# Optimization experiments

Measured on AMD Instinct MI355X. Metric: run time of the kernel, lower is better.

The kernel has to match this reference:

```python
import jax, jax.numpy as jnp
import numpy as np

B, L, C = 2048, 2048, 16
F = L // 2                 # num_freqs = 1024
H = 4 * F                  # multi_factor * num_freqs = 4096
P = int(len(np.unique(L // np.arange(1, F + 1))))  # n patch sizes = 88
SCALE = 0.02
NOISE_EPS = 0.01


def setup_inputs() -> dict:
    key = jax.random.key(0)
    ks = jax.random.split(key, 10)
    return {
        "x": jax.random.normal(ks[0], (B, L, C), jnp.float32),
        "w_start": SCALE * jax.random.normal(ks[1], (C, 1), jnp.float32),
        "b_start": SCALE * jax.random.normal(ks[2], (1,), jnp.float32),
        "w1": SCALE * jax.random.normal(ks[3], (2, F, H), jnp.float32),
        "b1": SCALE * jax.random.normal(ks[4], (2, H), jnp.float32),
        "w2": SCALE * jax.random.normal(ks[5], (2, H, F), jnp.float32),
        "b2": SCALE * jax.random.normal(ks[6], (2, F), jnp.float32),
        "w_gate": SCALE * jax.random.normal(ks[7], (F, P), jnp.float32),
        "w_noise": SCALE * jax.random.normal(ks[8], (F, P), jnp.float32),
        "noise_z": jax.random.normal(ks[9], (B, P), jnp.float32),
        "top_k": 3,
    }


def reference(x, w_start, b_start, w1, b1, w2, b2, w_gate, w_noise, noise_z, top_k):
    # start_fc: [B, L, C] -> [B, L, 1] -> [B, 1, L]
    v = (jnp.einsum("blc,co->blo", x, w_start) + b_start).transpose(0, 2, 1)
    # rfft (ortho), drop DC bin -> [B, 1, F] complex
    xf = jnp.fft.rfft(v, axis=-1, norm="ortho")[:, :, 1:]
    xr, xi = jnp.real(xf), jnp.imag(xf)
    # complex 2-layer MLP in frequency domain
    o1r = jax.nn.relu(jnp.einsum("bdi,io->bdo", xr, w1[0]) - jnp.einsum("bdi,io->bdo", xi, w1[1]) + b1[0])
    o1i = jax.nn.relu(jnp.einsum("bdi,io->bdo", xi, w1[0]) + jnp.einsum("bdi,io->bdo", xr, w1[1]) + b1[1])
    o2r = jnp.einsum("bdo,of->bdf", o1r, w2[0]) - jnp.einsum("bdo,of->bdf", o1i, w2[1]) + b2[0]
    o2i = jnp.einsum("bdo,of->bdf", o1i, w2[0]) + jnp.einsum("bdo,of->bdf", o1r, w2[1]) + b2[1]
    amp = jnp.sqrt(o2r * o2r + o2i * o2i)[:, 0, :]  # [B, F]
    # router logits with (training) noise injection
    clean_logits = amp @ w_gate                      # [B, P]
    noise_std = jax.nn.softplus(amp @ w_noise) + NOISE_EPS
    logits = clean_logits + noise_z * noise_std
    # top-k -> softmax over top-k -> scatter into sparse gates
    top_w, top_i = jax.lax.top_k(logits, top_k)
    top_w = jax.nn.softmax(top_w, axis=-1)
    rows = jnp.arange(logits.shape[0])[:, None]
    gates = jnp.zeros_like(logits).at[rows, top_i].set(top_w)
    return gates
```

## Files before the change

kernel.cpp:

```cpp
#include <hip/hip_runtime.h>
#include <hip/hip_bf16.h>
#include <math.h>

#define B_DIM 2048
#define L_DIM 2048
#define F_DIM 1024
#define H_DIM 4096
#define P_DIM 88

typedef unsigned short u16;
typedef short bf16x8 __attribute__((ext_vector_type(8)));
typedef float f32x4 __attribute__((ext_vector_type(4)));

__device__ __forceinline__ u16 f2bf(float x) {
    unsigned u = __float_as_uint(x);
    return (u16)((u + 0x7fffu + ((u >> 16) & 1u)) >> 16);
}
__device__ __forceinline__ float bf2f(u16 h) {
    return __uint_as_float(((unsigned)h) << 16);
}

__device__ __forceinline__ void gload_lds16(const void* g, void* l) {
    unsigned loff = (unsigned)(uintptr_t)l;
    __builtin_amdgcn_global_load_lds(
        reinterpret_cast<const __attribute__((address_space(1))) void*>(
            reinterpret_cast<uintptr_t>(g)),
        reinterpret_cast<__attribute__((address_space(3))) void*>(loff),
        16, 0, 0);
}

__global__ __launch_bounds__(256) void fft_kernel(
    const float* __restrict__ x, const float* __restrict__ w_start,
    const float* __restrict__ b_start, u16* __restrict__ A1)
{
    __shared__ float re[2048];
    __shared__ float im[2048];
    int b = blockIdx.x;

    const float4* wp = (const float4*)w_start;
    float4 w0 = wp[0], w1 = wp[1], w2 = wp[2], w3 = wp[3];
    float bs = b_start[0];

    for (int l = threadIdx.x; l < 2048; l += 256) {
        const float4* xp = (const float4*)(x + ((size_t)b * 2048 + l) * 16);
        float4 x0 = xp[0], x1 = xp[1], x2 = xp[2], x3 = xp[3];
        float acc = bs;
        acc += x0.x * w0.x + x0.y * w0.y + x0.z * w0.z + x0.w * w0.w;
        acc += x1.x * w1.x + x1.y * w1.y + x1.z * w1.z + x1.w * w1.w;
        acc += x2.x * w2.x + x2.y * w2.y + x2.z * w2.z + x2.w * w2.w;
        acc += x3.x * w3.x + x3.y * w3.y + x3.z * w3.z + x3.w * w3.w;
        unsigned j = __brev((unsigned)l) >> 21;
        re[j] = acc;
        im[j] = 0.f;
    }
    __syncthreads();

    for (int s = 1; s <= 11; s++) {
        int half = 1 << (s - 1);
        for (int t = threadIdx.x; t < 1024; t += 256) {
            int j = t & (half - 1);
            int base = (t >> (s - 1)) << s;
            float ang = -6.283185307179586f * (float)j / (float)(1 << s);
            float wr, wi;
            sincosf(ang, &wi, &wr);
            int i0 = base + j, i1 = i0 + half;
            float br = re[i1], bi = im[i1];
            float tr = br * wr - bi * wi;
            float ti = br * wi + bi * wr;
            float ar = re[i0], ai = im[i0];
            re[i0] = ar + tr; im[i0] = ai + ti;
            re[i1] = ar - tr; im[i1] = ai - ti;
        }
        __syncthreads();
    }

    const float sc = 0.022097086912079612f;
    u16* arow = A1 + (size_t)b * 4096;
    for (int t = threadIdx.x; t < 1024; t += 256) {
        float r = re[t + 1] * sc;
        float q = im[t + 1] * sc;
        u16 rh = f2bf(r); u16 rl = f2bf(r - bf2f(rh));
        u16 ih = f2bf(q); u16 il = f2bf(q - bf2f(ih));
        arow[t] = rh; arow[1024 + t] = rl;
        arow[2048 + t] = ih; arow[3072 + t] = il;
    }
}

__global__ __launch_bounds__(256) void conv_bt_kernel(
    const float* __restrict__ w, u16* __restrict__ BT, int Kc, int Nh)
{
    __shared__ float t0[32][33];
    __shared__ float t1[32][33];
    int k0 = blockIdx.x * 32, n0 = blockIdx.y * 32;
    int tx = threadIdx.x, ty = threadIdx.y;
    const float* w0 = w;
    const float* w1 = w + (size_t)Kc * Nh;

#pragma unroll
    for (int i = 0; i < 4; i++) {
        int k = k0 + ty + 8 * i;
        t0[ty + 8 * i][tx] = w0[(size_t)k * Nh + n0 + tx];
        t1[ty + 8 * i][tx] = w1[(size_t)k * Nh + n0 + tx];
    }
    __syncthreads();

    size_t K4 = 4 * (size_t)Kc;
    int k = k0 + tx;
#pragma unroll
    for (int i = 0; i < 4; i++) {
        int nl = ty + 8 * i;
        int n = n0 + nl;
        float br = t0[tx][nl];
        float bi = t1[tx][nl];
        u16 brh = f2bf(br); u16 brl = f2bf(br - bf2f(brh));
        float nbi = -bi;
        u16 nih = f2bf(nbi); u16 nil = f2bf(nbi - bf2f(nih));
        u16 pih = f2bf(bi);  u16 pil = f2bf(bi - bf2f(pih));
        u16* rowr = BT + (size_t)n * K4;
        rowr[0 * Kc + k] = brh; rowr[1 * Kc + k] = brl;
        rowr[2 * Kc + k] = nih; rowr[3 * Kc + k] = nil;
        u16* rowi = BT + (size_t)(Nh + n) * K4;
        rowi[0 * Kc + k] = pih; rowi[1 * Kc + k] = pil;
        rowi[2 * Kc + k] = brh; rowi[3 * Kc + k] = brl;
    }
}

extern __shared__ char smem8p[];

#define MFMA16(ACC0, ACC1, ACC2, ACC3, A0, A1, A2, A3)                          \
    ACC0[0] = __builtin_amdgcn_mfma_f32_16x16x32_bf16(A0, b0, ACC0[0], 0, 0, 0); \
    ACC0[1] = __builtin_amdgcn_mfma_f32_16x16x32_bf16(A0, b1, ACC0[1], 0, 0, 0); \
    ACC0[2] = __builtin_amdgcn_mfma_f32_16x16x32_bf16(A0, b2, ACC0[2], 0, 0, 0); \
    ACC0[3] = __builtin_amdgcn_mfma_f32_16x16x32_bf16(A0, b3, ACC0[3], 0, 0, 0); \
    ACC1[0] = __builtin_amdgcn_mfma_f32_16x16x32_bf16(A1, b0, ACC1[0], 0, 0, 0); \
    ACC1[1] = __builtin_amdgcn_mfma_f32_16x16x32_bf16(A1, b1, ACC1[1], 0, 0, 0); \
    ACC1[2] = __builtin_amdgcn_mfma_f32_16x16x32_bf16(A1, b2, ACC1[2], 0, 0, 0); \
    ACC1[3] = __builtin_amdgcn_mfma_f32_16x16x32_bf16(A1, b3, ACC1[3], 0, 0, 0); \
    ACC2[0] = __builtin_amdgcn_mfma_f32_16x16x32_bf16(A2, b0, ACC2[0], 0, 0, 0); \
    ACC2[1] = __builtin_amdgcn_mfma_f32_16x16x32_bf16(A2, b1, ACC2[1], 0, 0, 0); \
    ACC2[2] = __builtin_amdgcn_mfma_f32_16x16x32_bf16(A2, b2, ACC2[2], 0, 0, 0); \
    ACC2[3] = __builtin_amdgcn_mfma_f32_16x16x32_bf16(A2, b3, ACC2[3], 0, 0, 0); \
    ACC3[0] = __builtin_amdgcn_mfma_f32_16x16x32_bf16(A3, b0, ACC3[0], 0, 0, 0); \
    ACC3[1] = __builtin_amdgcn_mfma_f32_16x16x32_bf16(A3, b1, ACC3[1], 0, 0, 0); \
    ACC3[2] = __builtin_amdgcn_mfma_f32_16x16x32_bf16(A3, b2, ACC3[2], 0, 0, 0); \
    ACC3[3] = __builtin_amdgcn_mfma_f32_16x16x32_bf16(A3, b3, ACC3[3], 0, 0, 0);

template <int EPI, int SWZ>
__global__ __launch_bounds__(512, 2) void gemm8p(
    const u16* __restrict__ A, const u16* __restrict__ B,
    const float* __restrict__ biasL, const float* __restrict__ biasR,
    u16* __restrict__ OutU, float* __restrict__ P01, float* __restrict__ P23,
    int Kc, int KcLog, int NH, int nt)
{
    char* ldsA = smem8p;
    char* ldsB = smem8p + 65536;

    const int tid = threadIdx.x;
    const int w = tid >> 6, lane = tid & 63;
    const int wr = w >> 2, wc = w & 3;
    const int fr = lane & 15, kb = lane >> 4;

    int bx, by, z;
    if (SWZ) {
        int b = blockIdx.x;
        int xcd = b & 7, idx = b >> 3;
        bx = 4 * xcd + (idx & 3);
        by = idx >> 2;
        z = 0;
    } else {
        bx = blockIdx.x; by = blockIdx.y; z = blockIdx.z;
    }
    const int n0 = bx * 256, m0 = by * 256;
    const size_t K4 = 4 * (size_t)Kc;

    const int srow = tid >> 2;
    const int lk8 = (((tid & 3) ^ ((tid >> 3) & 3))) * 8;
    const int wb = (tid >> 6) * 1024;

    const int laneOff = fr * 64 + ((kb ^ ((fr >> 1) & 3)) << 4);

    f32x4 acc[8][4];
#pragma unroll
    for (int i = 0; i < 8; i++)
#pragma unroll
        for (int j = 0; j < 4; j++)
            acc[i][j] = (f32x4){0.f, 0.f, 0.f, 0.f};

    const int t0 = z * nt, te = t0 + nt;

    auto colA = [&](int t) {
        int k0 = t << 5;
        int seg = k0 >> KcLog, kk = k0 & (Kc - 1);
        int r3 = seg >= 3 ? seg - 3 : seg;
        int bs = seg >= 3 ? 2 : 0;
        return (bs + (r3 == 1 ? 1 : 0)) * Kc + kk;
    };
    auto colB = [&](int t) {
        int k0 = t << 5;
        int seg = k0 >> KcLog, kk = k0 & (Kc - 1);
        int r3 = seg >= 3 ? seg - 3 : seg;
        int bs = seg >= 3 ? 2 : 0;
        return (bs + (r3 == 2 ? 1 : 0)) * Kc + kk;
    };
    auto stageA = [&](int t) {
        const u16* src = A + (size_t)(m0 + srow) * K4 + colA(t) + lk8;
        char* dst = ldsA + (t & 3) * 16384 + wb;
        gload_lds16(src, dst);
        gload_lds16(src + (size_t)128 * K4, dst + 8192);
    };
    auto stageB = [&](int t) {
        const u16* src = B + (size_t)(n0 + srow) * K4 + colB(t) + lk8;
        char* dst = ldsB + (t & 3) * 16384 + wb;
        gload_lds16(src, dst);
        gload_lds16(src + (size_t)128 * K4, dst + 8192);
    };
    auto aBase = [&](int t) -> const char* {
        return ldsA + (t & 3) * 16384 + wr * 8192 + laneOff;
    };
    auto bBase = [&](int t) -> const char* {
        return ldsB + (t & 3) * 16384 + wc * 4096 + laneOff;
    };

    stageA(t0); stageB(t0);
    if (t0 + 1 < te) { stageA(t0 + 1); stageB(t0 + 1); }
    if (t0 + 1 < te) asm volatile("s_waitcnt vmcnt(4)" ::: "memory");
    else             asm volatile("s_waitcnt vmcnt(0)" ::: "memory");
    asm volatile("s_barrier" ::: "memory");

    bf16x8 b0, b1, b2, b3, a0, a1, a2, a3;
    {
        const char* aS = aBase(t0);
        const char* bS = bBase(t0);
        b0 = *(const bf16x8*)(bS + 0 * 1024);
        b1 = *(const bf16x8*)(bS + 1 * 1024);
        b2 = *(const bf16x8*)(bS + 2 * 1024);
        b3 = *(const bf16x8*)(bS + 3 * 1024);
        a0 = *(const bf16x8*)(aS + 0 * 1024);
        a1 = *(const bf16x8*)(aS + 1 * 1024);
        a2 = *(const bf16x8*)(aS + 2 * 1024);
        a3 = *(const bf16x8*)(aS + 3 * 1024);
    }

    for (int t = t0; t < te; ++t) {
        if (t + 2 < te) { stageA(t + 2); stageB(t + 2); }

        __builtin_amdgcn_s_setprio(1);
        MFMA16(acc[0], acc[1], acc[2], acc[3], a0, a1, a2, a3)
        __builtin_amdgcn_s_setprio(0);

        const char* aS = aBase(t);
        bf16x8 c0 = *(const bf16x8*)(aS + 4096 + 0 * 1024);
        bf16x8 c1 = *(const bf16x8*)(aS + 4096 + 1 * 1024);
        bf16x8 c2 = *(const bf16x8*)(aS + 4096 + 2 * 1024);
        bf16x8 c3 = *(const bf16x8*)(aS + 4096 + 3 * 1024);

        if (t + 2 < te) asm volatile("s_waitcnt vmcnt(4)" ::: "memory");
        else            asm volatile("s_waitcnt vmcnt(0)" ::: "memory");
        asm volatile("s_barrier" ::: "memory");

        __builtin_amdgcn_s_setprio(1);
        MFMA16(acc[4], acc[5], acc[6], acc[7], c0, c1, c2, c3)
        __builtin_amdgcn_s_setprio(0);

        if (t + 1 < te) {
            const char* aN = aBase(t + 1);
            const char* bN = bBase(t + 1);
            b0 = *(const bf16x8*)(bN + 0 * 1024);
            b1 = *(const bf16x8*)(bN + 1 * 1024);
            b2 = *(const bf16x8*)(bN + 2 * 1024);
            b3 = *(const bf16x8*)(bN + 3 * 1024);
            a0 = *(const bf16x8*)(aN + 0 * 1024);
            a1 = *(const bf16x8*)(aN + 1 * 1024);
            a2 = *(const bf16x8*)(aN + 2 * 1024);
            a3 = *(const bf16x8*)(aN + 3 * 1024);
        }
    }

    const int fq = kb;
#pragma unroll
    for (int nj = 0; nj < 4; nj++) {
        int n = n0 + wc * 64 + nj * 16 + fr;
        if (EPI == 0) {
            bool left = (n < NH);
            int nn = left ? n : (n - NH);
            float bias = left ? biasL[n] : biasR[nn];
#pragma unroll
            for (int mi = 0; mi < 8; mi++) {
                int mb = m0 + wr * 128 + mi * 16 + fq * 4;
#pragma unroll
                for (int r = 0; r < 4; r++) {
                    float val = fmaxf(acc[mi][nj][r] + bias, 0.f);
                    u16 h = f2bf(val);
                    u16 lo = f2bf(val - bf2f(h));
                    size_t rb = (size_t)(mb + r) * (4 * (size_t)NH);
                    if (left) { OutU[rb + nn] = h; OutU[rb + NH + nn] = lo; }
                    else { OutU[rb + 2 * (size_t)NH + nn] = h; OutU[rb + 3 * (size_t)NH + nn] = lo; }
                }
            }
        } else {
            const size_t PSZ = (size_t)2048 * 2048;
            float* Out = (z < 2) ? (P01 + (size_t)z * PSZ) : (P23 + (size_t)(z - 2) * PSZ);
#pragma unroll
            for (int mi = 0; mi < 8; mi++) {
                int mb = m0 + wr * 128 + mi * 16 + fq * 4;
#pragma unroll
                for (int r = 0; r < 4; r++)
                    Out[(size_t)(mb + r) * 2048 + n] = acc[mi][nj][r];
            }
        }
    }
}

__global__ __launch_bounds__(128) void router_kernel(
    const float* __restrict__ P01, const float* __restrict__ P23, int ZK,
    const float* __restrict__ b2,
    const float* __restrict__ w_gate, const float* __restrict__ w_noise,
    const float* __restrict__ noise_z, float* __restrict__ gates)
{
    __shared__ float s_amp[1024];
    __shared__ float s_logit[P_DIM];
    __shared__ int   s_idx[3];
    __shared__ float s_val[3];

    int b = blockIdx.x;
    const size_t PSZ = (size_t)2048 * 2048;
    const size_t roff = (size_t)b * 2048;

    for (int i = threadIdx.x; i < 1024; i += 128) {
        float orr = b2[i];
        float oii = b2[1024 + i];
        for (int zz = 0; zz < ZK; zz++) {
            const float* Pz = ((zz < 2) ? (P01 + (size_t)zz * PSZ)
                                        : (P23 + (size_t)(zz - 2) * PSZ)) + roff;
            orr += Pz[i];
            oii += Pz[1024 + i];
        }
        s_amp[i] = sqrtf(orr * orr + oii * oii);
    }
    __syncthreads();

    int p = threadIdx.x;
    if (p < P_DIM) {
        float cg = 0.f, cn = 0.f;
        for (int k = 0; k < 1024; k++) {
            float a = s_amp[k];
            cg = fmaf(a, w_gate[k * P_DIM + p], cg);
            cn = fmaf(a, w_noise[k * P_DIM + p], cn);
        }
        float ns = (cn > 20.f) ? cn : log1pf(expf(cn));
        ns += 0.01f;
        s_logit[p] = cg + noise_z[(size_t)b * P_DIM + p] * ns;
    }
    __syncthreads();

    if (threadIdx.x == 0) {
        int i0 = -1, i1 = -1, i2 = -1;
        float v0 = -1e30f, v1 = -1e30f, v2 = -1e30f;
        for (int i = 0; i < P_DIM; i++) {
            float t = s_logit[i];
            if (t > v0) { v0 = t; i0 = i; }
        }
        for (int i = 0; i < P_DIM; i++) {
            if (i == i0) continue;
            float t = s_logit[i];
            if (t > v1) { v1 = t; i1 = i; }
        }
        for (int i = 0; i < P_DIM; i++) {
            if (i == i0 || i == i1) continue;
            float t = s_logit[i];
            if (t > v2) { v2 = t; i2 = i; }
        }
        s_idx[0] = i0; s_idx[1] = i1; s_idx[2] = i2;
        s_val[0] = v0; s_val[1] = v1; s_val[2] = v2;
    }
    __syncthreads();

    if (p < P_DIM) {
        float m = s_val[0];
        float e0 = expf(s_val[0] - m);
        float e1 = expf(s_val[1] - m);
        float e2 = expf(s_val[2] - m);
        float inv = 1.f / (e0 + e1 + e2);
        float g = 0.f;
        if (p == s_idx[0]) g = e0 * inv;
        else if (p == s_idx[1]) g = e1 * inv;
        else if (p == s_idx[2]) g = e2 * inv;
        gates[(size_t)b * P_DIM + p] = g;
    }
}

extern "C" void kernel_launch(void* const* d_in, const int* in_sizes, int n_in,
                              void* d_out, int out_size, void* d_ws, size_t ws_size,
                              hipStream_t stream)
{
    const float* x       = (const float*)d_in[0];
    const float* w_start = (const float*)d_in[1];
    const float* b_start = (const float*)d_in[2];
    const float* w1      = (const float*)d_in[3];
    const float* b1      = (const float*)d_in[4];
    const float* w2      = (const float*)d_in[5];
    const float* b2      = (const float*)d_in[6];
    const float* w_gate  = (const float*)d_in[7];
    const float* w_noise = (const float*)d_in[8];
    const float* noise_z = (const float*)d_in[9];
    float* gates = (float*)d_out;

    const size_t MB = 1024 * 1024;
    char* base = (char*)d_ws;
    u16*  A1   = (u16*)(base + 16 * MB);
    u16*  BT   = (u16*)(base + 32 * MB);
    u16*  A2   = (u16*)(base + 96 * MB);
    float* P01 = (float*)base;
    float* P23 = (float*)(base + 160 * MB);

    int ZK = (ws_size >= (size_t)192 * MB) ? 4 : 2;

    hipFuncSetAttribute(reinterpret_cast<const void*>(&gemm8p<0, 1>),
                        hipFuncAttributeMaxDynamicSharedMemorySize, 131072);
    hipFuncSetAttribute(reinterpret_cast<const void*>(&gemm8p<1, 0>),
                        hipFuncAttributeMaxDynamicSharedMemorySize, 131072);

    fft_kernel<<<B_DIM, 256, 0, stream>>>(x, w_start, b_start, A1);

    conv_bt_kernel<<<dim3(F_DIM / 32, H_DIM / 32), dim3(32, 8), 0, stream>>>(
        w1, BT, F_DIM, H_DIM);
    gemm8p<0, 1><<<256, 512, 131072, stream>>>(
        A1, BT, b1, b1 + H_DIM, A2, nullptr, nullptr, F_DIM, 10, H_DIM, 192);

    conv_bt_kernel<<<dim3(H_DIM / 32, F_DIM / 32), dim3(32, 8), 0, stream>>>(
        w2, BT, H_DIM, F_DIM);
    gemm8p<1, 0><<<dim3(8, 8, ZK), 512, 131072, stream>>>(
        A2, BT, nullptr, nullptr, nullptr, P01, P23, H_DIM, 12, F_DIM, 768 / ZK);

    router_kernel<<<B_DIM, 128, 0, stream>>>(
        P01, P23, ZK, b2, w_gate, w_noise, noise_z, gates);
}
```

Measured before the change: 595.5 us.

## Restructure GEMM main loop to 64-wide K steps with double-buffered LDS halves

The bf16 MFMA GEMM now processes 64 K-elements per iteration, split into two 32-wide LDS sub-stages in a double buffer, replacing the 4-deep ring of 32-wide stages. The next tile's halves are prefetched while the current ones are consumed, halving loop trip counts and barrier frequency per K unit. Staging addresses are precomputed per wave and the fragment loads are reorganized. The FFT kernel also precomputes twiddle factors in shared memory once instead of calling sincos in every butterfly stage.

```diff
diff --git a/kernel.cpp b/kernel.cpp
--- a/kernel.cpp
+++ b/kernel.cpp
@@ -35,11 +35,18 @@
 {
     __shared__ float re[2048];
     __shared__ float im[2048];
+    __shared__ float twr[1024];
+    __shared__ float twi[1024];
     int b = blockIdx.x;
 
     const float4* wp = (const float4*)w_start;
     float4 w0 = wp[0], w1 = wp[1], w2 = wp[2], w3 = wp[3];
     float bs = b_start[0];
+
+    for (int i = threadIdx.x; i < 1024; i += 256) {
+        float ang = -6.283185307179586f * ((float)i / 2048.0f);
+        sincosf(ang, &twi[i], &twr[i]);
+    }
 
     for (int l = threadIdx.x; l < 2048; l += 256) {
         const float4* xp = (const float4*)(x + ((size_t)b * 2048 + l) * 16);
@@ -60,9 +67,8 @@
         for (int t = threadIdx.x; t < 1024; t += 256) {
             int j = t & (half - 1);
             int base = (t >> (s - 1)) << s;
-            float ang = -6.283185307179586f * (float)j / (float)(1 << s);
-            float wr, wi;
-            sincosf(ang, &wi, &wr);
+            int idx = j << (11 - s);
+            float wr = twr[idx], wi = twi[idx];
             int i0 = base + j, i1 = i0 + half;
             float br = re[i1], bi = im[i1];
             float tr = br * wr - bi * wi;
@@ -127,23 +133,23 @@
 
 extern __shared__ char smem8p[];
 
-#define MFMA16(ACC0, ACC1, ACC2, ACC3, A0, A1, A2, A3)                          \
-    ACC0[0] = __builtin_amdgcn_mfma_f32_16x16x32_bf16(A0, b0, ACC0[0], 0, 0, 0); \
-    ACC0[1] = __builtin_amdgcn_mfma_f32_16x16x32_bf16(A0, b1, ACC0[1], 0, 0, 0); \
-    ACC0[2] = __builtin_amdgcn_mfma_f32_16x16x32_bf16(A0, b2, ACC0[2], 0, 0, 0); \
-    ACC0[3] = __builtin_amdgcn_mfma_f32_16x16x32_bf16(A0, b3, ACC0[3], 0, 0, 0); \
-    ACC1[0] = __builtin_amdgcn_mfma_f32_16x16x32_bf16(A1, b0, ACC1[0], 0, 0, 0); \
-    ACC1[1] = __builtin_amdgcn_mfma_f32_16x16x32_bf16(A1, b1, ACC1[1], 0, 0, 0); \
-    ACC1[2] = __builtin_amdgcn_mfma_f32_16x16x32_bf16(A1, b2, ACC1[2], 0, 0, 0); \
-    ACC1[3] = __builtin_amdgcn_mfma_f32_16x16x32_bf16(A1, b3, ACC1[3], 0, 0, 0); \
-    ACC2[0] = __builtin_amdgcn_mfma_f32_16x16x32_bf16(A2, b0, ACC2[0], 0, 0, 0); \
-    ACC2[1] = __builtin_amdgcn_mfma_f32_16x16x32_bf16(A2, b1, ACC2[1], 0, 0, 0); \
-    ACC2[2] = __builtin_amdgcn_mfma_f32_16x16x32_bf16(A2, b2, ACC2[2], 0, 0, 0); \
-    ACC2[3] = __builtin_amdgcn_mfma_f32_16x16x32_bf16(A2, b3, ACC2[3], 0, 0, 0); \
-    ACC3[0] = __builtin_amdgcn_mfma_f32_16x16x32_bf16(A3, b0, ACC3[0], 0, 0, 0); \
-    ACC3[1] = __builtin_amdgcn_mfma_f32_16x16x32_bf16(A3, b1, ACC3[1], 0, 0, 0); \
-    ACC3[2] = __builtin_amdgcn_mfma_f32_16x16x32_bf16(A3, b2, ACC3[2], 0, 0, 0); \
-    ACC3[3] = __builtin_amdgcn_mfma_f32_16x16x32_bf16(A3, b3, ACC3[3], 0, 0, 0);
+#define MFMA_PHASE(MB, A0_, A1_, A2_, A3_, B0_, B1_, B2_, B3_)                        \
+    acc[MB+0][0] = __builtin_amdgcn_mfma_f32_16x16x32_bf16(A0_, B0_, acc[MB+0][0],0,0,0); \
+    acc[MB+0][1] = __builtin_amdgcn_mfma_f32_16x16x32_bf16(A0_, B1_, acc[MB+0][1],0,0,0); \
+    acc[MB+0][2] = __builtin_amdgcn_mfma_f32_16x16x32_bf16(A0_, B2_, acc[MB+0][2],0,0,0); \
+    acc[MB+0][3] = __builtin_amdgcn_mfma_f32_16x16x32_bf16(A0_, B3_, acc[MB+0][3],0,0,0); \
+    acc[MB+1][0] = __builtin_amdgcn_mfma_f32_16x16x32_bf16(A1_, B0_, acc[MB+1][0],0,0,0); \
+    acc[MB+1][1] = __builtin_amdgcn_mfma_f32_16x16x32_bf16(A1_, B1_, acc[MB+1][1],0,0,0); \
+    acc[MB+1][2] = __builtin_amdgcn_mfma_f32_16x16x32_bf16(A1_, B2_, acc[MB+1][2],0,0,0); \
+    acc[MB+1][3] = __builtin_amdgcn_mfma_f32_16x16x32_bf16(A1_, B3_, acc[MB+1][3],0,0,0); \
+    acc[MB+2][0] = __builtin_amdgcn_mfma_f32_16x16x32_bf16(A2_, B0_, acc[MB+2][0],0,0,0); \
+    acc[MB+2][1] = __builtin_amdgcn_mfma_f32_16x16x32_bf16(A2_, B1_, acc[MB+2][1],0,0,0); \
+    acc[MB+2][2] = __builtin_amdgcn_mfma_f32_16x16x32_bf16(A2_, B2_, acc[MB+2][2],0,0,0); \
+    acc[MB+2][3] = __builtin_amdgcn_mfma_f32_16x16x32_bf16(A2_, B3_, acc[MB+2][3],0,0,0); \
+    acc[MB+3][0] = __builtin_amdgcn_mfma_f32_16x16x32_bf16(A3_, B0_, acc[MB+3][0],0,0,0); \
+    acc[MB+3][1] = __builtin_amdgcn_mfma_f32_16x16x32_bf16(A3_, B1_, acc[MB+3][1],0,0,0); \
+    acc[MB+3][2] = __builtin_amdgcn_mfma_f32_16x16x32_bf16(A3_, B2_, acc[MB+3][2],0,0,0); \
+    acc[MB+3][3] = __builtin_amdgcn_mfma_f32_16x16x32_bf16(A3_, B3_, acc[MB+3][3],0,0,0);
 
 template <int EPI, int SWZ>
 __global__ __launch_bounds__(512, 2) void gemm8p(
@@ -152,9 +158,6 @@
     u16* __restrict__ OutU, float* __restrict__ P01, float* __restrict__ P23,
     int Kc, int KcLog, int NH, int nt)
 {
-    char* ldsA = smem8p;
-    char* ldsB = smem8p + 65536;
-
     const int tid = threadIdx.x;
     const int w = tid >> 6, lane = tid & 63;
     const int wr = w >> 2, wc = w & 3;
@@ -173,11 +176,22 @@
     const int n0 = bx * 256, m0 = by * 256;
     const size_t K4 = 4 * (size_t)Kc;
 
-    const int srow = tid >> 2;
-    const int lk8 = (((tid & 3) ^ ((tid >> 3) & 3))) * 8;
-    const int wb = (tid >> 6) * 1024;
-
-    const int laneOff = fr * 64 + ((kb ^ ((fr >> 1) & 3)) << 4);
+    const int srow = lane >> 2;
+    const int pch  = lane & 3;
+    const int rU0 = w * 32 + srow;
+    const int rU1 = rU0 + 16;
+    const int e0 = (pch ^ ((rU0 >> 1) & 3)) * 8;
+    const int e1 = (pch ^ ((rU1 >> 1) & 3)) * 8;
+    const u16* gA0 = A + (size_t)(m0 + rU0) * K4 + e0;
+    const u16* gA1 = A + (size_t)(m0 + rU1) * K4 + e1;
+    const u16* gB0 = B + (size_t)(n0 + rU0) * K4 + e0;
+    const u16* gB1 = B + (size_t)(n0 + rU1) * K4 + e1;
+    const int dU0 = (w * 32) * 64;
+    const int dU1 = dU0 + 16 * 64;
+
+    const int xk   = (kb ^ ((fr >> 1) & 3)) << 4;
+    const int aOff = (wr * 128 + fr) * 64 + xk;
+    const int bOff = 16384 + (wc * 64 + fr) * 64 + xk;
 
     f32x4 acc[8][4];
 #pragma unroll
@@ -186,94 +200,91 @@
         for (int j = 0; j < 4; j++)
             acc[i][j] = (f32x4){0.f, 0.f, 0.f, 0.f};
 
-    const int t0 = z * nt, te = t0 + nt;
-
     auto colA = [&](int t) {
-        int k0 = t << 5;
+        int k0 = t << 6;
         int seg = k0 >> KcLog, kk = k0 & (Kc - 1);
         int r3 = seg >= 3 ? seg - 3 : seg;
         int bs = seg >= 3 ? 2 : 0;
         return (bs + (r3 == 1 ? 1 : 0)) * Kc + kk;
     };
     auto colB = [&](int t) {
-        int k0 = t << 5;
+        int k0 = t << 6;
         int seg = k0 >> KcLog, kk = k0 & (Kc - 1);
         int r3 = seg >= 3 ? seg - 3 : seg;
         int bs = seg >= 3 ? 2 : 0;
         return (bs + (r3 == 2 ? 1 : 0)) * Kc + kk;
     };
-    auto stageA = [&](int t) {
-        const u16* src = A + (size_t)(m0 + srow) * K4 + colA(t) + lk8;
-        char* dst = ldsA + (t & 3) * 16384 + wb;
-        gload_lds16(src, dst);
-        gload_lds16(src + (size_t)128 * K4, dst + 8192);
+    auto stageK = [&](int t, int ks) {
+        char* d = smem8p + ((t & 1) << 16) + (ks << 15);
+        int cA = colA(t) + ks * 32;
+        int cB = colB(t) + ks * 32;
+        gload_lds16(gA0 + cA, d + dU0);
+        gload_lds16(gA1 + cA, d + dU1);
+        gload_lds16(gB0 + cB, d + 16384 + dU0);
+        gload_lds16(gB1 + cB, d + 16384 + dU1);
     };
-    auto stageB = [&](int t) {
-        const u16* src = B + (size_t)(n0 + srow) * K4 + colB(t) + lk8;
-        char* dst = ldsB + (t & 3) * 16384 + wb;
-        gload_lds16(src, dst);
-        gload_lds16(src + (size_t)128 * K4, dst + 8192);
-    };
-    auto aBase = [&](int t) -> const char* {
-        return ldsA + (t & 3) * 16384 + wr * 8192 + laneOff;
-    };
-    auto bBase = [&](int t) -> const char* {
-        return ldsB + (t & 3) * 16384 + wc * 4096 + laneOff;
-    };
-
-    stageA(t0); stageB(t0);
-    if (t0 + 1 < te) { stageA(t0 + 1); stageB(t0 + 1); }
-    if (t0 + 1 < te) asm volatile("s_waitcnt vmcnt(4)" ::: "memory");
-    else             asm volatile("s_waitcnt vmcnt(0)" ::: "memory");
+
+    const int t0 = z * nt, te = t0 + nt;
+
+    stageK(t0, 0);
+    stageK(t0, 1);
+    asm volatile("s_waitcnt vmcnt(4)" ::: "memory");
     asm volatile("s_barrier" ::: "memory");
 
-    bf16x8 b0, b1, b2, b3, a0, a1, a2, a3;
-    {
-        const char* aS = aBase(t0);
-        const char* bS = bBase(t0);
-        b0 = *(const bf16x8*)(bS + 0 * 1024);
-        b1 = *(const bf16x8*)(bS + 1 * 1024);
-        b2 = *(const bf16x8*)(bS + 2 * 1024);
-        b3 = *(const bf16x8*)(bS + 3 * 1024);
-        a0 = *(const bf16x8*)(aS + 0 * 1024);
-        a1 = *(const bf16x8*)(aS + 1 * 1024);
-        a2 = *(const bf16x8*)(aS + 2 * 1024);
-        a3 = *(const bf16x8*)(aS + 3 * 1024);
-    }
-
     for (int t = t0; t < te; ++t) {
-        if (t + 2 < te) { stageA(t + 2); stageB(t + 2); }
-
+        const char* sl = smem8p + ((t & 1) << 16);
+        const char* aP = sl + aOff;
+        const char* bP = sl + bOff;
+        const bool more = (t + 1 < te);
+
+        bf16x8 a0 = *(const bf16x8*)(aP + 0 * 1024);
+        bf16x8 a1 = *(const bf16x8*)(aP + 1 * 1024);
+        bf16x8 a2 = *(const bf16x8*)(aP + 2 * 1024);
+        bf16x8 a3 = *(const bf16x8*)(aP + 3 * 1024);
+        bf16x8 b0 = *(const bf16x8*)(bP + 0 * 1024);
+        bf16x8 b1 = *(const bf16x8*)(bP + 1 * 1024);
+        bf16x8 b2 = *(const bf16x8*)(bP + 2 * 1024);
+        bf16x8 b3 = *(const bf16x8*)(bP + 3 * 1024);
+        if (more) stageK(t + 1, 0);
         __builtin_amdgcn_s_setprio(1);
-        MFMA16(acc[0], acc[1], acc[2], acc[3], a0, a1, a2, a3)
+        MFMA_PHASE(0, a0, a1, a2, a3, b0, b1, b2, b3)
         __builtin_amdgcn_s_setprio(0);
 
-        const char* aS = aBase(t);
-        bf16x8 c0 = *(const bf16x8*)(aS + 4096 + 0 * 1024);
-        bf16x8 c1 = *(const bf16x8*)(aS + 4096 + 1 * 1024);
-        bf16x8 c2 = *(const bf16x8*)(aS + 4096 + 2 * 1024);
-        bf16x8 c3 = *(const bf16x8*)(aS + 4096 + 3 * 1024);
-
-        if (t + 2 < te) asm volatile("s_waitcnt vmcnt(4)" ::: "memory");
-        else            asm volatile("s_waitcnt vmcnt(0)" ::: "memory");
+        a0 = *(const bf16x8*)(aP + 4 * 1024);
+        a1 = *(const bf16x8*)(aP + 5 * 1024);
+        a2 = *(const bf16x8*)(aP + 6 * 1024);
+        a3 = *(const bf16x8*)(aP + 7 * 1024);
+        __builtin_amdgcn_s_setprio(1);
+        MFMA_PHASE(4, a0, a1, a2, a3, b0, b1, b2, b3)
+        __builtin_amdgcn_s_setprio(0);
+        if (more) asm volatile("s_waitcnt vmcnt(4)" ::: "memory");
+        else      asm volatile("s_waitcnt vmcnt(0)" ::: "memory");
         asm volatile("s_barrier" ::: "memory");
 
+        const char* aQ = aP + 32768;
+        const char* bQ = bP + 32768;
+        a0 = *(const bf16x8*)(aQ + 0 * 1024);
+        a1 = *(const bf16x8*)(aQ + 1 * 1024);
+        a2 = *(const bf16x8*)(aQ + 2 * 1024);
+        a3 = *(const bf16x8*)(aQ + 3 * 1024);
+        b0 = *(const bf16x8*)(bQ + 0 * 1024);
+        b1 = *(const bf16x8*)(bQ + 1 * 1024);
+        b2 = *(const bf16x8*)(bQ + 2 * 1024);
+        b3 = *(const bf16x8*)(bQ + 3 * 1024);
+        if (more) stageK(t + 1, 1);
         __builtin_amdgcn_s_setprio(1);
-        MFMA16(acc[4], acc[5], acc[6], acc[7], c0, c1, c2, c3)
+        MFMA_PHASE(0, a0, a1, a2, a3, b0, b1, b2, b3)
         __builtin_amdgcn_s_setprio(0);
 
-        if (t + 1 < te) {
-            const char* aN = aBase(t + 1);
-            const char* bN = bBase(t + 1);
-            b0 = *(const bf16x8*)(bN + 0 * 1024);
-            b1 = *(const bf16x8*)(bN + 1 * 1024);
-            b2 = *(const bf16x8*)(bN + 2 * 1024);
-            b3 = *(const bf16x8*)(bN + 3 * 1024);
-            a0 = *(const bf16x8*)(aN + 0 * 1024);
-            a1 = *(const bf16x8*)(aN + 1 * 1024);
-            a2 = *(const bf16x8*)(aN + 2 * 1024);
-            a3 = *(const bf16x8*)(aN + 3 * 1024);
-        }
+        a0 = *(const bf16x8*)(aQ + 4 * 1024);
+        a1 = *(const bf16x8*)(aQ + 5 * 1024);
+        a2 = *(const bf16x8*)(aQ + 6 * 1024);
+        a3 = *(const bf16x8*)(aQ + 7 * 1024);
+        __builtin_amdgcn_s_setprio(1);
+        MFMA_PHASE(4, a0, a1, a2, a3, b0, b1, b2, b3)
+        __builtin_amdgcn_s_setprio(0);
+        if (more) asm volatile("s_waitcnt vmcnt(4)" ::: "memory");
+        asm volatile("s_barrier" ::: "memory");
     }
 
     const int fq = kb;
@@ -425,12 +436,12 @@
     conv_bt_kernel<<<dim3(F_DIM / 32, H_DIM / 32), dim3(32, 8), 0, stream>>>(
         w1, BT, F_DIM, H_DIM);
     gemm8p<0, 1><<<256, 512, 131072, stream>>>(
-        A1, BT, b1, b1 + H_DIM, A2, nullptr, nullptr, F_DIM, 10, H_DIM, 192);
+        A1, BT, b1, b1 + H_DIM, A2, nullptr, nullptr, F_DIM, 10, H_DIM, 96);
 
     conv_bt_kernel<<<dim3(H_DIM / 32, F_DIM / 32), dim3(32, 8), 0, stream>>>(
         w2, BT, H_DIM, F_DIM);
     gemm8p<1, 0><<<dim3(8, 8, ZK), 512, 131072, stream>>>(
-        A2, BT, nullptr, nullptr, nullptr, P01, P23, H_DIM, 12, F_DIM, 768 / ZK);
+        A2, BT, nullptr, nullptr, nullptr, P01, P23, H_DIM, 12, F_DIM, 384 / ZK);
 
     router_kernel<<<B_DIM, 128, 0, stream>>>(
         P01, P23, ZK, b2, w_gate, w_noise, noise_z, gates);
```

After: 600.5 us. Within noise of the previous version (+0.8%).
